# Kernel tuning notes

Hardware: AMD Instinct MI355X
Metric: run time of the kernel (lower is better)

## Reference

```python
import jax, jax.numpy as jnp
from jax import lax
import numpy as np

B, T = 64, 2048
RNN_DIM, EMB_DIM, ATT_DIM = 1024, 512, 128
N_FILT, KSIZE = 32, 31
PAD = (KSIZE - 1) // 2


def setup_inputs() -> dict:
    key = jax.random.key(0)
    ks = jax.random.split(key, 10)
    attention_hidden_state = jax.random.normal(ks[0], (B, RNN_DIM), dtype=jnp.float32)
    memory = jax.random.normal(ks[1], (B, T, EMB_DIM), dtype=jnp.float32)
    processed_memory = jax.random.normal(ks[2], (B, T, ATT_DIM), dtype=jnp.float32)
    attention_weights = jax.random.uniform(ks[3], (B, T), dtype=jnp.float32)
    attention_weights_cum = jax.random.uniform(ks[4], (B, T), dtype=jnp.float32)
    mask = jnp.zeros((B, T), dtype=bool)  # no padding -> all positions valid
    # learned params
    Wq = jax.random.normal(ks[5], (ATT_DIM, RNN_DIM), dtype=jnp.float32) / np.sqrt(RNN_DIM)
    conv_w = jax.random.normal(ks[6], (N_FILT, 2, KSIZE), dtype=jnp.float32) / np.sqrt(2 * KSIZE)
    Wd = jax.random.normal(ks[7], (ATT_DIM, N_FILT), dtype=jnp.float32) / np.sqrt(N_FILT)
    Wv = jax.random.normal(ks[8], (ATT_DIM,), dtype=jnp.float32) / np.sqrt(ATT_DIM)
    return {
        'attention_hidden_state': attention_hidden_state,
        'memory': memory,
        'processed_memory': processed_memory,
        'attention_weights': attention_weights,
        'attention_weights_cum': attention_weights_cum,
        'Wq': Wq, 'conv_w': conv_w, 'Wd': Wd, 'Wv': Wv,
        'mask': mask,
    }


def reference(attention_hidden_state, memory, processed_memory,
              attention_weights, attention_weights_cum,
              Wq, conv_w, Wd, Wv, mask):
    # processed query: (B, ATT_DIM), broadcast over time
    pq = attention_hidden_state @ Wq.T  # (B, D)
    # location features: conv over [prev, cumulative] attention weights
    cat = jnp.stack([attention_weights, attention_weights_cum], axis=1)  # (B, 2, T)
    loc = lax.conv_general_dilated(
        cat, conv_w, window_strides=(1,), padding=[(PAD, PAD)],
        dimension_numbers=('NCH', 'OIH', 'NCH'))  # (B, F, T)
    loc = jnp.einsum('bft,df->btd', loc, Wd)  # (B, T, D)
    # additive energies
    energies = jnp.einsum('btd,d->bt', jnp.tanh(pq[:, None, :] + loc + processed_memory), Wv)
    energies = jnp.where(mask, -jnp.inf, energies)
    w = jax.nn.softmax(energies, axis=1)  # (B, T)
    context = jnp.einsum('bt,bte->be', w, memory)  # (B, EMB_DIM)
    return context
```

## Files before the change

### kernel.cpp

```cpp
#include <hip/hip_runtime.h>

#define BB 64
#define TT 2048
#define RNN_DIM 1024
#define EMB_DIM 512
#define ATT_DIM 128
#define N_FILT 32
#define KSIZE 31
#define PADW 15
#define CK 62

__device__ __align__(16) float g_pq[BB * ATT_DIM];
__device__ __align__(16) float g_W2[ATT_DIM * 64];
__device__ __align__(16) float g_e[BB * TT];
__device__ float g_sm[BB];
__device__ float g_sinv[BB];

__global__ __launch_bounds__(256) void prep_kernel(const float* __restrict__ hidden,
                                                   const float* __restrict__ Wq,
                                                   const float* __restrict__ conv_w,
                                                   const float* __restrict__ Wd,
                                                   float* __restrict__ out) {
    const int tid = threadIdx.x;
    if (blockIdx.x < BB) {
        const int b = blockIdx.x;
        __shared__ __align__(16) float h_s[RNN_DIM];
        ((float4*)h_s)[tid] = ((const float4*)(hidden + b * RNN_DIM))[tid];
        __syncthreads();
        const int d = tid >> 1;
        const int hh = tid & 1;
        const float4* wrow = (const float4*)(Wq + d * RNN_DIM) + hh * 128;
        const float4* hv = ((const float4*)h_s) + hh * 128;
        float s = 0.f;
        #pragma unroll 8
        for (int j = 0; j < 128; j++) {
            float4 wv = wrow[j];
            float4 hx = hv[j];
            s += wv.x * hx.x + wv.y * hx.y + wv.z * hx.z + wv.w * hx.w;
        }
        s += __shfl_xor(s, 1, 64);
        if (hh == 0) g_pq[b * ATT_DIM + d] = s;
    } else if (blockIdx.x == BB) {
        for (int idx = tid; idx < ATT_DIM * 64; idx += 256) {
            int d = idx >> 6;
            int ck = idx & 63;
            float s = 0.f;
            if (ck < CK) {
                int c = ck / KSIZE;
                int k = ck % KSIZE;
                #pragma unroll
                for (int f = 0; f < N_FILT; f++)
                    s += Wd[d * N_FILT + f] * conv_w[(f * 2 + c) * KSIZE + k];
            }
            g_W2[idx] = s;
        }
    } else {
        const int z = blockIdx.x - BB - 1;
        float4* o4 = (float4*)out;
        #pragma unroll
        for (int i = 0; i < 16; i++) {
            float4 zz = {0.f, 0.f, 0.f, 0.f};
            o4[z * 4096 + i * 256 + tid] = zz;
        }
    }
}

__global__ __launch_bounds__(256) void energy_kernel(const float* __restrict__ pm,
                                                     const float* __restrict__ aw,
                                                     const float* __restrict__ awc,
                                                     const float* __restrict__ Wv) {
    const int b = blockIdx.y;
    const int t0 = blockIdx.x * 64;
    const int tid = threadIdx.x;
    const int lane = tid & 63;

    __shared__ __align__(16) float pm_s[64 * 129];
    __shared__ float cat_s[2][64 + 2 * PADW];
    __shared__ float part_s[4][64];

    {
        const int c4 = tid & 31;
        const int trow = tid >> 5;
        #pragma unroll
        for (int p = 0; p < 8; p++) {
            const int tl = trow + 8 * p;
            float4 v = ((const float4*)(pm + ((size_t)(b * TT + t0 + tl)) * ATT_DIM))[c4];
            *((float4*)(pm_s + tl * 129 + 4 * c4)) = v;
        }
    }
    for (int i = tid; i < 64 + 2 * PADW; i += 256) {
        int g = t0 - PADW + i;
        bool ok = (g >= 0) && (g < TT);
        cat_s[0][i] = ok ? aw[b * TT + g] : 0.f;
        cat_s[1][i] = ok ? awc[b * TT + g] : 0.f;
    }
    __syncthreads();

    float win0[KSIZE], win1[KSIZE];
    #pragma unroll
    for (int k = 0; k < KSIZE; k++) {
        win0[k] = cat_s[0][lane + k];
        win1[k] = cat_s[1][lane + k];
    }

    const int w_u = __builtin_amdgcn_readfirstlane(tid >> 6);
    float e_acc = 0.f;
    #pragma unroll 2
    for (int dd = 0; dd < 32; dd++) {
        const int d = w_u * 32 + dd;
        const float* w2r = g_W2 + d * 64;
        float c0 = 0.f, c1 = 0.f;
        #pragma unroll
        for (int k = 0; k < KSIZE; k++) c0 += w2r[k] * win0[k];
        #pragma unroll
        for (int k = 0; k < KSIZE; k++) c1 += w2r[31 + k] * win1[k];
        float s = g_pq[b * ATT_DIM + d] + pm_s[lane * 129 + d] + c0 + c1;
        float th = 1.f - 2.f / (1.f + __expf(2.f * s));
        e_acc += Wv[d] * th;
    }
    part_s[w_u][lane] = e_acc;
    __syncthreads();
    if (tid < 64) {
        float e = part_s[0][tid] + part_s[1][tid] + part_s[2][tid] + part_s[3][tid];
        g_e[b * TT + t0 + tid] = e;
    }
}

__global__ __launch_bounds__(256) void rowstat_kernel() {
    const int b = blockIdx.x;
    const int tid = threadIdx.x;
    const int wid = tid >> 6, lane = tid & 63;
    __shared__ float red_s[8];
    float ev[8];
    #pragma unroll
    for (int i = 0; i < 8; i++) ev[i] = g_e[b * TT + tid + 256 * i];
    float m = ev[0];
    #pragma unroll
    for (int i = 1; i < 8; i++) m = fmaxf(m, ev[i]);
    #pragma unroll
    for (int off = 32; off > 0; off >>= 1) m = fmaxf(m, __shfl_xor(m, off, 64));
    if (lane == 0) red_s[wid] = m;
    __syncthreads();
    m = fmaxf(fmaxf(red_s[0], red_s[1]), fmaxf(red_s[2], red_s[3]));
    float s = 0.f;
    #pragma unroll
    for (int i = 0; i < 8; i++) s += __expf(ev[i] - m);
    #pragma unroll
    for (int off = 32; off > 0; off >>= 1) s += __shfl_xor(s, off, 64);
    __syncthreads();
    if (lane == 0) red_s[4 + wid] = s;
    __syncthreads();
    if (tid == 0) {
        g_sm[b] = m;
        g_sinv[b] = 1.f / (red_s[4] + red_s[5] + red_s[6] + red_s[7]);
    }
}

__global__ __launch_bounds__(256) void context_kernel(const float* __restrict__ memory,
                                                      float* __restrict__ out) {
    const int b = blockIdx.y;
    const int t0 = blockIdx.x * 128;
    const int tid = threadIdx.x;
    const int f4 = tid & 127;
    const int tg = tid >> 7;
    __shared__ float w_s[128];
    __shared__ __align__(16) float4 ctx_s[128];
    if (tid < 128) {
        float m = g_sm[b], inv = g_sinv[b];
        w_s[tid] = __expf(g_e[b * TT + t0 + tid] - m) * inv;
    }
    __syncthreads();
    float4 acc = {0.f, 0.f, 0.f, 0.f};
    for (int i = tg; i < 128; i += 2) {
        float wv = w_s[i];
        float4 mv = ((const float4*)(memory + ((size_t)(b * TT + t0 + i)) * EMB_DIM))[f4];
        acc.x += wv * mv.x; acc.y += wv * mv.y;
        acc.z += wv * mv.z; acc.w += wv * mv.w;
    }
    if (tg == 1) ctx_s[f4] = acc;
    __syncthreads();
    if (tg == 0) {
        float4 o = ctx_s[f4];
        float* op = out + b * EMB_DIM + 4 * f4;
        atomicAdd(op + 0, acc.x + o.x);
        atomicAdd(op + 1, acc.y + o.y);
        atomicAdd(op + 2, acc.z + o.z);
        atomicAdd(op + 3, acc.w + o.w);
    }
}

extern "C" void kernel_launch(void* const* d_in, const int* in_sizes, int n_in,
                              void* d_out, int out_size, void* d_ws, size_t ws_size,
                              hipStream_t stream) {
    const float* hidden = (const float*)d_in[0];
    const float* memory = (const float*)d_in[1];
    const float* pm     = (const float*)d_in[2];
    const float* aw     = (const float*)d_in[3];
    const float* awc    = (const float*)d_in[4];
    const float* Wq     = (const float*)d_in[5];
    const float* conv_w = (const float*)d_in[6];
    const float* Wd     = (const float*)d_in[7];
    const float* Wv     = (const float*)d_in[8];
    float* out = (float*)d_out;

    prep_kernel<<<dim3(BB + 3), 256, 0, stream>>>(hidden, Wq, conv_w, Wd, out);
    energy_kernel<<<dim3(TT / 64, BB), 256, 0, stream>>>(pm, aw, awc, Wv);
    rowstat_kernel<<<dim3(BB), 256, 0, stream>>>();
    context_kernel<<<dim3(TT / 128, BB), 256, 0, stream>>>(memory, out);
}
```

Baseline: 483.4 us.

## Factor location conv through filters, fuse softmax partial stats into energy kernel

The energy kernel no longer applies a precomputed 128x62 combined conv/projection matrix per time step. It first computes the 32 conv filter outputs into shared memory, then projects them with Wd, cutting per-element FMAs from about 62 to 32 per attention dim. The energy kernel also emits per-block max/sum partials, so rowstat becomes a single block merging 32 partials per row instead of rereading all energies. The Wq projection is split over 4x more blocks for parallelism. This adds an extra shared-memory pass and a sync inside the energy kernel.

```diff
diff --git a/kernel.cpp b/kernel.cpp
--- a/kernel.cpp
+++ b/kernel.cpp
@@ -8,66 +8,53 @@
 #define N_FILT 32
 #define KSIZE 31
 #define PADW 15
-#define CK 62
 
 __device__ __align__(16) float g_pq[BB * ATT_DIM];
-__device__ __align__(16) float g_W2[ATT_DIM * 64];
 __device__ __align__(16) float g_e[BB * TT];
+__device__ float g_pmax[BB * 32];
+__device__ float g_psum[BB * 32];
 __device__ float g_sm[BB];
 __device__ float g_sinv[BB];
 
 __global__ __launch_bounds__(256) void prep_kernel(const float* __restrict__ hidden,
                                                    const float* __restrict__ Wq,
-                                                   const float* __restrict__ conv_w,
-                                                   const float* __restrict__ Wd,
                                                    float* __restrict__ out) {
     const int tid = threadIdx.x;
-    if (blockIdx.x < BB) {
-        const int b = blockIdx.x;
+    if (blockIdx.x < 256) {
+        const int b = blockIdx.x >> 2;
+        const int dq = (blockIdx.x & 3) * 32;
         __shared__ __align__(16) float h_s[RNN_DIM];
         ((float4*)h_s)[tid] = ((const float4*)(hidden + b * RNN_DIM))[tid];
         __syncthreads();
-        const int d = tid >> 1;
-        const int hh = tid & 1;
-        const float4* wrow = (const float4*)(Wq + d * RNN_DIM) + hh * 128;
-        const float4* hv = ((const float4*)h_s) + hh * 128;
+        const int dl = tid >> 3;
+        const int hh = tid & 7;
+        const int d = dq + dl;
+        const float4* wrow = (const float4*)(Wq + d * RNN_DIM) + hh * 32;
+        const float4* hv = ((const float4*)h_s) + hh * 32;
         float s = 0.f;
         #pragma unroll 8
-        for (int j = 0; j < 128; j++) {
+        for (int j = 0; j < 32; j++) {
             float4 wv = wrow[j];
             float4 hx = hv[j];
             s += wv.x * hx.x + wv.y * hx.y + wv.z * hx.z + wv.w * hx.w;
         }
         s += __shfl_xor(s, 1, 64);
+        s += __shfl_xor(s, 2, 64);
+        s += __shfl_xor(s, 4, 64);
         if (hh == 0) g_pq[b * ATT_DIM + d] = s;
-    } else if (blockIdx.x == BB) {
-        for (int idx = tid; idx < ATT_DIM * 64; idx += 256) {
-            int d = idx >> 6;
-            int ck = idx & 63;
-            float s = 0.f;
-            if (ck < CK) {
-                int c = ck / KSIZE;
-                int k = ck % KSIZE;
-                #pragma unroll
-                for (int f = 0; f < N_FILT; f++)
-                    s += Wd[d * N_FILT + f] * conv_w[(f * 2 + c) * KSIZE + k];
-            }
-            g_W2[idx] = s;
-        }
     } else {
-        const int z = blockIdx.x - BB - 1;
         float4* o4 = (float4*)out;
-        #pragma unroll
-        for (int i = 0; i < 16; i++) {
-            float4 zz = {0.f, 0.f, 0.f, 0.f};
-            o4[z * 4096 + i * 256 + tid] = zz;
-        }
+        float4 zz = {0.f, 0.f, 0.f, 0.f};
+        #pragma unroll
+        for (int i = 0; i < 32; i++) o4[i * 256 + tid] = zz;
     }
 }
 
 __global__ __launch_bounds__(256) void energy_kernel(const float* __restrict__ pm,
                                                      const float* __restrict__ aw,
                                                      const float* __restrict__ awc,
+                                                     const float* __restrict__ conv_w,
+                                                     const float* __restrict__ Wd,
                                                      const float* __restrict__ Wv) {
     const int b = blockIdx.y;
     const int t0 = blockIdx.x * 64;
@@ -76,6 +63,7 @@
 
     __shared__ __align__(16) float pm_s[64 * 129];
     __shared__ float cat_s[2][64 + 2 * PADW];
+    __shared__ float locF_s[64 * 33];
     __shared__ float part_s[4][64];
 
     {
@@ -104,17 +92,33 @@
     }
 
     const int w_u = __builtin_amdgcn_readfirstlane(tid >> 6);
+
+    #pragma unroll
+    for (int j = 0; j < 8; j++) {
+        const int f = w_u * 8 + j;
+        const float* cw = conv_w + f * 62;
+        float c0 = 0.f, c1 = 0.f;
+        #pragma unroll
+        for (int k = 0; k < KSIZE; k++) c0 += cw[k] * win0[k];
+        #pragma unroll
+        for (int k = 0; k < KSIZE; k++) c1 += cw[31 + k] * win1[k];
+        locF_s[lane * 33 + f] = c0 + c1;
+    }
+    __syncthreads();
+
+    float lf[N_FILT];
+    #pragma unroll
+    for (int f = 0; f < N_FILT; f++) lf[f] = locF_s[lane * 33 + f];
+
     float e_acc = 0.f;
     #pragma unroll 2
     for (int dd = 0; dd < 32; dd++) {
         const int d = w_u * 32 + dd;
-        const float* w2r = g_W2 + d * 64;
-        float c0 = 0.f, c1 = 0.f;
-        #pragma unroll
-        for (int k = 0; k < KSIZE; k++) c0 += w2r[k] * win0[k];
-        #pragma unroll
-        for (int k = 0; k < KSIZE; k++) c1 += w2r[31 + k] * win1[k];
-        float s = g_pq[b * ATT_DIM + d] + pm_s[lane * 129 + d] + c0 + c1;
+        const float* wd = Wd + d * N_FILT;
+        float p = 0.f;
+        #pragma unroll
+        for (int f = 0; f < N_FILT; f++) p += wd[f] * lf[f];
+        float s = g_pq[b * ATT_DIM + d] + pm_s[lane * 129 + d] + p;
         float th = 1.f - 2.f / (1.f + __expf(2.f * s));
         e_acc += Wv[d] * th;
     }
@@ -123,36 +127,40 @@
     if (tid < 64) {
         float e = part_s[0][tid] + part_s[1][tid] + part_s[2][tid] + part_s[3][tid];
         g_e[b * TT + t0 + tid] = e;
+        float m = e;
+        #pragma unroll
+        for (int off = 32; off > 0; off >>= 1) m = fmaxf(m, __shfl_xor(m, off, 64));
+        float x = __expf(e - m);
+        #pragma unroll
+        for (int off = 32; off > 0; off >>= 1) x += __shfl_xor(x, off, 64);
+        if (tid == 0) {
+            g_pmax[b * 32 + blockIdx.x] = m;
+            g_psum[b * 32 + blockIdx.x] = x;
+        }
     }
 }
 
 __global__ __launch_bounds__(256) void rowstat_kernel() {
-    const int b = blockIdx.x;
-    const int tid = threadIdx.x;
-    const int wid = tid >> 6, lane = tid & 63;
-    __shared__ float red_s[8];
-    float ev[8];
-    #pragma unroll
-    for (int i = 0; i < 8; i++) ev[i] = g_e[b * TT + tid + 256 * i];
-    float m = ev[0];
-    #pragma unroll
-    for (int i = 1; i < 8; i++) m = fmaxf(m, ev[i]);
-    #pragma unroll
-    for (int off = 32; off > 0; off >>= 1) m = fmaxf(m, __shfl_xor(m, off, 64));
-    if (lane == 0) red_s[wid] = m;
-    __syncthreads();
-    m = fmaxf(fmaxf(red_s[0], red_s[1]), fmaxf(red_s[2], red_s[3]));
-    float s = 0.f;
-    #pragma unroll
-    for (int i = 0; i < 8; i++) s += __expf(ev[i] - m);
-    #pragma unroll
-    for (int off = 32; off > 0; off >>= 1) s += __shfl_xor(s, off, 64);
-    __syncthreads();
-    if (lane == 0) red_s[4 + wid] = s;
-    __syncthreads();
-    if (tid == 0) {
+    const int tid = threadIdx.x;
+    const int b = tid >> 2, q = tid & 3;
+    float ms[8], ss[8];
+    float m = -1e30f;
+    #pragma unroll
+    for (int i = 0; i < 8; i++) {
+        ms[i] = g_pmax[b * 32 + q * 8 + i];
+        ss[i] = g_psum[b * 32 + q * 8 + i];
+        m = fmaxf(m, ms[i]);
+    }
+    m = fmaxf(m, __shfl_xor(m, 1, 64));
+    m = fmaxf(m, __shfl_xor(m, 2, 64));
+    float z = 0.f;
+    #pragma unroll
+    for (int i = 0; i < 8; i++) z += ss[i] * __expf(ms[i] - m);
+    z += __shfl_xor(z, 1, 64);
+    z += __shfl_xor(z, 2, 64);
+    if (q == 0) {
         g_sm[b] = m;
-        g_sinv[b] = 1.f / (red_s[4] + red_s[5] + red_s[6] + red_s[7]);
+        g_sinv[b] = 1.f / z;
     }
 }
 
@@ -203,8 +211,8 @@
     const float* Wv     = (const float*)d_in[8];
     float* out = (float*)d_out;
 
-    prep_kernel<<<dim3(BB + 3), 256, 0, stream>>>(hidden, Wq, conv_w, Wd, out);
-    energy_kernel<<<dim3(TT / 64, BB), 256, 0, stream>>>(pm, aw, awc, Wv);
-    rowstat_kernel<<<dim3(BB), 256, 0, stream>>>();
+    prep_kernel<<<dim3(257), 256, 0, stream>>>(hidden, Wq, out);
+    energy_kernel<<<dim3(TT / 64, BB), 256, 0, stream>>>(pm, aw, awc, conv_w, Wd, Wv);
+    rowstat_kernel<<<dim3(1), 256, 0, stream>>>();
     context_kernel<<<dim3(TT / 128, BB), 256, 0, stream>>>(memory, out);
 }
```

Result: faster. 457.8 us (-5.3%).
